# Performance work log

Measured on AMD Instinct MI355X. Metric: run time of the kernel, lower is better.

The kernel has to match this reference:

```python
import jax, jax.numpy as jnp
import numpy as np

V = 10000
C = 8192
NC = 64        # num_clusters
SPW = 128      # states_per_word
H = 256        # hidden_dim
B = 16
T = 33
NEG = -1.0e30  # stand-in for -inf to keep log_softmax NaN-free on empty rows


def residual(x, w1, b1, w2, b2):
    # ResidualLayer: relu(lin2(relu(lin1(x)))) + x  (dropout=0 / eval mode)
    h = jax.nn.relu(x @ w1.T + b1)
    return jax.nn.relu(h @ w2.T + b2) + x


def setup_inputs() -> dict:
    key = jax.random.key(0)
    ks = jax.random.split(key, 32)
    s = 0.02

    def p(k, shape):
        return jax.random.normal(k, shape, jnp.float32) * s

    inp = {}
    inp['text'] = jax.random.randint(ks[0], (B, T), 0, V)
    # brown-cluster style assignment: each cluster owns a contiguous block of SPW states
    word2cluster = jax.random.randint(ks[1], (V,), 0, NC)
    cluster2state = jnp.arange(NC * SPW).reshape(NC, SPW)  # [NC, SPW]
    inp['word2state'] = cluster2state[word2cluster]        # [V, SPW]

    inp['start_emb'] = p(ks[2], (C, H))
    inp['sw1'] = p(ks[3], (H, H)); inp['sb1'] = jnp.zeros((H,), jnp.float32)
    inp['sw2'] = p(ks[4], (H, H)); inp['sb2'] = jnp.zeros((H,), jnp.float32)
    inp['sow'] = p(ks[5], (1, H)); inp['sob'] = jnp.zeros((1,), jnp.float32)

    inp['state_emb'] = p(ks[6], (C, H))
    inp['tw1'] = p(ks[7], (H, H)); inp['tb1'] = jnp.zeros((H,), jnp.float32)
    inp['tw2'] = p(ks[8], (H, H)); inp['tb2'] = jnp.zeros((H,), jnp.float32)
    inp['next_state_emb'] = p(ks[9], (C, H))

    inp['preterminal_emb'] = p(ks[10], (C, H))
    inp['ew1'] = p(ks[11], (H, H)); inp['eb1'] = jnp.zeros((H,), jnp.float32)
    inp['ew2'] = p(ks[12], (H, H)); inp['eb2'] = jnp.zeros((H,), jnp.float32)
    inp['proj_w'] = p(ks[13], (V, H)); inp['proj_b'] = jnp.zeros((V,), jnp.float32)
    return inp


def reference(text, word2state,
              start_emb, sw1, sb1, sw2, sb2, sow, sob,
              state_emb, tw1, tb1, tw2, tb2, next_state_emb,
              preterminal_emb, ew1, eb1, ew2, eb2, proj_w, proj_b):
    # ---- start distribution over C states ----
    start = jax.nn.log_softmax(
        (residual(start_emb, sw1, sb1, sw2, sb2) @ sow.T + sob).squeeze(-1))  # [C]
    # ---- transition [C, C] ----
    trans_logits = residual(state_emb, tw1, tb1, tw2, tb2) @ next_state_emb.T
    transition = jax.nn.log_softmax(trans_logits, axis=-1)  # [C, C]
    # ---- masked emission [C, V] ----
    logits = residual(preterminal_emb, ew1, eb1, ew2, eb2) @ proj_w.T + proj_b
    mask = jnp.zeros((C, V), bool).at[
        word2state.reshape(-1), jnp.repeat(jnp.arange(V), SPW)].set(True)
    emission = jax.nn.log_softmax(jnp.where(mask, logits, NEG), axis=-1)  # [C, V]

    # ---- clamp: gather per-token factored potentials ----
    cs = word2state[text]  # [B, T, SPW]
    lp = transition[cs[:, :-1, :, None], cs[:, 1:, None, :]]  # [B, T-1, SPW(prev), SPW(next)]
    init = start[cs[:, 0]]                                     # [B, SPW]
    obs = emission[cs, text[:, :, None]]                       # [B, T, SPW]
    lp = lp + obs[:, 1:, None, :]                  # obs at t+1 broadcast over prev
    lp = lp.at[:, 0].add(init[:, :, None] + obs[:, 0, :, None])
    lp = lp.swapaxes(-1, -2)  # [B, T-1, next, prev] (as in clamp's final transpose)

    # ---- HMM forward recursion (evidence), the fb kernel's core scan ----
    alpha = jax.nn.logsumexp(lp[:, 0], axis=-1)  # [B, SPW]
    def step(a, lpt):
        # lpt: [B, next, prev]; a: [B, prev]
        return jax.nn.logsumexp(lpt + a[:, None, :], axis=-1), None
    alpha, _ = jax.lax.scan(step, alpha, lp[:, 1:].swapaxes(0, 1))
    return jax.nn.logsumexp(alpha, axis=-1)  # [B] log evidence
```

## Files before the change

### kernel.cpp

```cpp
#include <hip/hip_runtime.h>

#define CC 8192
#define VV 10000
#define NB 16
#define NT 33
#define NCL 64
#define TSCALE 5.545177444479562f

typedef float float4v __attribute__((ext_vector_type(4)));
typedef float f32x4 __attribute__((ext_vector_type(4)));
typedef _Float16 half8v __attribute__((ext_vector_type(8)));
typedef _Float16 half4v __attribute__((ext_vector_type(4)));

__global__ __launch_bounds__(256) void conv_f16(const float* __restrict__ A,
                                                _Float16* __restrict__ O, int n4) {
    int i = blockIdx.x * 256 + threadIdx.x;
    if (i >= n4) return;
    float4v a = ((const float4v*)A)[i];
    half4v h;
#pragma unroll
    for (int c = 0; c < 4; ++c) h[c] = (_Float16)a[c];
    ((half4v*)O)[i] = h;
}

__global__ __launch_bounds__(256) void conv_w6(const float* __restrict__ p0, const float* __restrict__ p1,
                                               const float* __restrict__ p2, const float* __restrict__ p3,
                                               const float* __restrict__ p4, const float* __restrict__ p5,
                                               _Float16* __restrict__ O) {
    const int w = blockIdx.y;
    const float* A = w == 0 ? p0 : w == 1 ? p1 : w == 2 ? p2 : w == 3 ? p3 : w == 4 ? p4 : p5;
    int i = blockIdx.x * 256 + threadIdx.x;
    float4v a = ((const float4v*)A)[i];
    half4v h;
#pragma unroll
    for (int c = 0; c < 4; ++c) h[c] = (_Float16)a[c];
    ((half4v*)(O + w * 65536))[i] = h;
}

__global__ __launch_bounds__(256) void conv2_f16(const float* __restrict__ A0, _Float16* __restrict__ O0, int n40,
                                                 const float* __restrict__ A1, _Float16* __restrict__ O1, int n41) {
    const float* A = blockIdx.y ? A1 : A0;
    _Float16* O = blockIdx.y ? O1 : O0;
    int n4 = blockIdx.y ? n41 : n40;
    int i = blockIdx.x * 256 + threadIdx.x;
    if (i >= n4) return;
    float4v a = ((const float4v*)A)[i];
    half4v h;
#pragma unroll
    for (int c = 0; c < 4; ++c) h[c] = (_Float16)a[c];
    ((half4v*)O)[i] = h;
}

template<bool RES, bool OUTF, bool OUTH>
__global__ __launch_bounds__(256) void mlp_f16(const _Float16* __restrict__ X,
                                               const _Float16* __restrict__ W,
                                               const float* __restrict__ bias,
                                               const float* __restrict__ Xres,
                                               float* __restrict__ Yf,
                                               _Float16* __restrict__ Yh) {
    __shared__ uint4 sB[1024];
    _Float16* BS = (_Float16*)sB;
    const int bm = blockIdx.x * 64;
    const int bn = blockIdx.y * 128;
    const int tid = threadIdx.x;
    const int w = tid >> 6, l = tid & 63;
    const int l15 = l & 15, l4 = l >> 4;
    half8v ax[8];
    {
        const size_t ro = (size_t)(bm + w * 16 + l15) * 256;
#pragma unroll
        for (int s = 0; s < 8; ++s)
            ax[s] = *(const half8v*)&X[ro + s * 32 + l4 * 8];
    }
    f32x4 acc[8];
#pragma unroll
    for (int ct = 0; ct < 8; ++ct) acc[ct] = (f32x4)0.f;
    for (int k0 = 0; k0 < 256; k0 += 64) {
        __syncthreads();
#pragma unroll
        for (int ii = 0; ii < 4; ++ii) {
            int L = ii * 256 + tid;
            int r = L >> 3, g = L & 7;
            int dst = r * 64 + ((g ^ (r & 7)) * 8);
            *(uint4*)&BS[dst] = *(const uint4*)&W[(size_t)(bn + r) * 256 + k0 + g * 8];
        }
        __syncthreads();
        const int sA = k0 >> 5;
#pragma unroll
        for (int ct = 0; ct < 8; ++ct) {
#pragma unroll
            for (int ks = 0; ks < 2; ++ks) {
                int r = ct * 16 + l15;
                int off = r * 64 + (((ks * 4 + l4) ^ (r & 7)) * 8);
                half8v bf = *(const half8v*)&BS[off];
                acc[ct] = __builtin_amdgcn_mfma_f32_16x16x32_f16(ax[sA + ks], bf, acc[ct], 0, 0, 0);
            }
        }
    }
#pragma unroll
    for (int ct = 0; ct < 8; ++ct) {
        int col = bn + ct * 16 + l15;
        float bv = bias[col];
#pragma unroll
        for (int q = 0; q < 4; ++q) {
            int row = bm + w * 16 + l4 * 4 + q;
            float v = acc[ct][q] + bv;
            v = v > 0.f ? v : 0.f;
            if (RES) v += Xres[(size_t)row * 256 + col];
            if (OUTF) Yf[(size_t)row * 256 + col] = v;
            if (OUTH) Yh[(size_t)row * 256 + col] = (_Float16)v;
        }
    }
}

__global__ __launch_bounds__(256) void trans_z_f16(const _Float16* __restrict__ E,
                                                   const _Float16* __restrict__ N,
                                                   float* __restrict__ Zpm,
                                                   float* __restrict__ Zps) {
    __shared__ uint4 sN[1024];
    _Float16* NS = (_Float16*)sN;
    const int bm = blockIdx.x * 128;
    const int cchunk = blockIdx.y;
    const int tid = threadIdx.x;
    const int w = tid >> 6, l = tid & 63;
    const int l15 = l & 15, l4 = l >> 4;
    half8v ax[2][8];
#pragma unroll
    for (int rt = 0; rt < 2; ++rt) {
        const size_t ro = (size_t)(bm + w * 32 + rt * 16 + l15) * 256;
#pragma unroll
        for (int s = 0; s < 8; ++s)
            ax[rt][s] = *(const half8v*)&E[ro + s * 32 + l4 * 8];
    }
    float rm[2][4], rs[2][4];
#pragma unroll
    for (int rt = 0; rt < 2; ++rt)
#pragma unroll
        for (int q = 0; q < 4; ++q) { rm[rt][q] = -1e30f; rs[rt][q] = 0.f; }

    for (int jt = 0; jt < 4; ++jt) {
        const int cb = cchunk * 512 + jt * 128;
        f32x4 acc[2][8];
#pragma unroll
        for (int rt = 0; rt < 2; ++rt)
#pragma unroll
            for (int ct = 0; ct < 8; ++ct) acc[rt][ct] = (f32x4)0.f;
        for (int k0 = 0; k0 < 256; k0 += 64) {
            __syncthreads();
#pragma unroll
            for (int ii = 0; ii < 4; ++ii) {
                int L = ii * 256 + tid;
                int r = L >> 3, g = L & 7;
                int dst = r * 64 + ((g ^ (r & 7)) * 8);
                *(uint4*)&NS[dst] = *(const uint4*)&N[(size_t)(cb + r) * 256 + k0 + g * 8];
            }
            __syncthreads();
            const int sA = k0 >> 5;
#pragma unroll
            for (int ct = 0; ct < 8; ++ct) {
#pragma unroll
                for (int ks = 0; ks < 2; ++ks) {
                    int r = ct * 16 + l15;
                    int off = r * 64 + (((ks * 4 + l4) ^ (r & 7)) * 8);
                    half8v nf = *(const half8v*)&NS[off];
                    acc[0][ct] = __builtin_amdgcn_mfma_f32_16x16x32_f16(ax[0][sA + ks], nf, acc[0][ct], 0, 0, 0);
                    acc[1][ct] = __builtin_amdgcn_mfma_f32_16x16x32_f16(ax[1][sA + ks], nf, acc[1][ct], 0, 0, 0);
                }
            }
        }
#pragma unroll
        for (int rt = 0; rt < 2; ++rt)
#pragma unroll
            for (int q = 0; q < 4; ++q) {
                float lm = -1e30f;
#pragma unroll
                for (int ct = 0; ct < 8; ++ct) lm = fmaxf(lm, acc[rt][ct][q]);
                lm = fmaxf(lm, __shfl_xor(lm, 1));
                lm = fmaxf(lm, __shfl_xor(lm, 2));
                lm = fmaxf(lm, __shfl_xor(lm, 4));
                lm = fmaxf(lm, __shfl_xor(lm, 8));
                float ls = 0.f;
#pragma unroll
                for (int ct = 0; ct < 8; ++ct) ls += __expf(acc[rt][ct][q] - lm);
                ls += __shfl_xor(ls, 1);
                ls += __shfl_xor(ls, 2);
                ls += __shfl_xor(ls, 4);
                ls += __shfl_xor(ls, 8);
                float nm = fmaxf(rm[rt][q], lm);
                rs[rt][q] = rs[rt][q] * __expf(rm[rt][q] - nm) + ls * __expf(lm - nm);
                rm[rt][q] = nm;
            }
    }
    if (l15 == 0) {
#pragma unroll
        for (int rt = 0; rt < 2; ++rt)
#pragma unroll
            for (int q = 0; q < 4; ++q) {
                int row = w * 32 + rt * 16 + l4 * 4 + q;
                Zpm[cchunk * CC + bm + row] = rm[rt][q];
                Zps[cchunk * CC + bm + row] = rs[rt][q];
            }
    }
}

__global__ __launch_bounds__(256) void z_combine(const float* __restrict__ Zpm,
                                                 const float* __restrict__ Zps,
                                                 float* __restrict__ Z) {
    const int i = blockIdx.x * 256 + threadIdx.x;
    float m = -1e30f;
#pragma unroll
    for (int c = 0; c < 16; ++c) m = fmaxf(m, Zpm[c * CC + i]);
    float s = 0.f;
#pragma unroll
    for (int c = 0; c < 16; ++c) s += Zps[c * CC + i] * __expf(Zpm[c * CC + i] - m);
    Z[i] = m + __logf(s);
}

__global__ __launch_bounds__(256) void g_blocks_f16(const _Float16* __restrict__ E,
                                                    const _Float16* __restrict__ N,
                                                    const float* __restrict__ Zt,
                                                    const int* __restrict__ text,
                                                    const int* __restrict__ wcl,
                                                    _Float16* __restrict__ T16) {
    const int bt = blockIdx.x;
    const int b = bt >> 5, t = bt & 31;
    const int ca = wcl[text[b * NT + t]];
    const int cb = wcl[text[b * NT + t + 1]];
    const int tid = threadIdx.x;
    const int w = tid >> 6, l = tid & 63;
    const int l15 = l & 15, l4 = l >> 4;
    half8v ax[2][8];
#pragma unroll
    for (int rt = 0; rt < 2; ++rt) {
        const size_t ro = (size_t)(ca * 128 + w * 32 + rt * 16 + l15) * 256;
#pragma unroll
        for (int s = 0; s < 8; ++s)
            ax[rt][s] = *(const half8v*)&E[ro + s * 32 + l4 * 8];
    }
    f32x4 acc[2][8];
#pragma unroll
    for (int rt = 0; rt < 2; ++rt)
#pragma unroll
        for (int ct = 0; ct < 8; ++ct) acc[rt][ct] = (f32x4)0.f;
#pragma unroll
    for (int s = 0; s < 8; ++s) {
#pragma unroll
        for (int ct = 0; ct < 8; ++ct) {
            half8v nf = *(const half8v*)&N[(size_t)(cb * 128 + ct * 16 + l15) * 256 + s * 32 + l4 * 8];
            acc[0][ct] = __builtin_amdgcn_mfma_f32_16x16x32_f16(ax[0][s], nf, acc[0][ct], 0, 0, 0);
            acc[1][ct] = __builtin_amdgcn_mfma_f32_16x16x32_f16(ax[1][s], nf, acc[1][ct], 0, 0, 0);
        }
    }
    _Float16* Gt = T16 + (size_t)bt * 16384;
#pragma unroll
    for (int rt = 0; rt < 2; ++rt)
#pragma unroll
        for (int q = 0; q < 4; ++q) {
            int row = w * 32 + rt * 16 + l4 * 4 + q;
            float z = Zt[ca * 128 + row];
#pragma unroll
            for (int ct = 0; ct < 8; ++ct)
                Gt[row * 128 + ct * 16 + l15] = (_Float16)__expf(acc[rt][ct][q] - z + TSCALE);
        }
}

__global__ __launch_bounds__(256) void wcl_k(const int* __restrict__ w2s, int* __restrict__ wcl) {
    int v = blockIdx.x * 256 + threadIdx.x;
    if (v < VV) wcl[v] = w2s[(size_t)v * 128] >> 7;
}

__global__ __launch_bounds__(64) void wlist_k(const int* __restrict__ wcl,
                                              int* __restrict__ wlist,
                                              int* __restrict__ cnt) {
    const int a = blockIdx.x;
    const int t = threadIdx.x;
    int c = 0;
    for (int base = 0; base < VV; base += 64) {
        int v = base + t;
        bool match = (v < VV) && (wcl[v] == a);
        unsigned long long mk = __ballot(match);
        if (match) {
            int pos = c + __popcll(mk & ((1ull << t) - 1ull));
            if (pos < 512) wlist[a * 512 + pos] = v;
        }
        c += __popcll(mk);
    }
    if (t == 0) cnt[a] = min(c, 512);
}

__global__ __launch_bounds__(64) void z_e_f16(const _Float16* __restrict__ Ep,
                                              const _Float16* __restrict__ Wp,
                                              const float* __restrict__ pb,
                                              const int* __restrict__ wlist,
                                              const int* __restrict__ cnt,
                                              float* __restrict__ Zem,
                                              float* __restrict__ Zes) {
    const int a = blockIdx.x, sg = blockIdx.y, wt = blockIdx.z;
    const int l = threadIdx.x, l15 = l & 15, l4 = l >> 4;
    const int n = cnt[a];
    const int orow = a * 128 + sg * 16;
    if (wt * 32 >= n) {
        if (l15 == 0) {
#pragma unroll
            for (int q = 0; q < 4; ++q) {
                int ro = orow + l4 * 4 + q;
                Zem[wt * CC + ro] = -1e30f;
                Zes[wt * CC + ro] = 0.f;
            }
        }
        return;
    }
    half8v ax[8];
    {
        const size_t ro = (size_t)(orow + l15) * 256;
#pragma unroll
        for (int s = 0; s < 8; ++s)
            ax[s] = *(const half8v*)&Ep[ro + s * 32 + l4 * 8];
    }
    float val[2][4];
#pragma unroll
    for (int ct = 0; ct < 2; ++ct) {
        const int wi = wt * 32 + ct * 16 + l15;
        const bool valid = wi < n;
        const int wrow = wlist[a * 512 + (valid ? wi : 0)];
        f32x4 acc = (f32x4)0.f;
        const size_t wo = (size_t)wrow * 256;
#pragma unroll
        for (int s = 0; s < 8; ++s) {
            half8v bf = *(const half8v*)&Wp[wo + s * 32 + l4 * 8];
            acc = __builtin_amdgcn_mfma_f32_16x16x32_f16(ax[s], bf, acc, 0, 0, 0);
        }
        const float pbv = valid ? pb[wrow] : 0.f;
#pragma unroll
        for (int q = 0; q < 4; ++q)
            val[ct][q] = valid ? (acc[q] + pbv) : -1e30f;
    }
#pragma unroll
    for (int q = 0; q < 4; ++q) {
        float m = fmaxf(val[0][q], val[1][q]);
        m = fmaxf(m, __shfl_xor(m, 1));
        m = fmaxf(m, __shfl_xor(m, 2));
        m = fmaxf(m, __shfl_xor(m, 4));
        m = fmaxf(m, __shfl_xor(m, 8));
        float s = __expf(val[0][q] - m) + __expf(val[1][q] - m);
        s += __shfl_xor(s, 1);
        s += __shfl_xor(s, 2);
        s += __shfl_xor(s, 4);
        s += __shfl_xor(s, 8);
        if (l15 == 0) {
            int ro = orow + l4 * 4 + q;
            Zem[wt * CC + ro] = m;
            Zes[wt * CC + ro] = s;
        }
    }
}

__global__ __launch_bounds__(256) void z_e_combine(const float* __restrict__ Zem,
                                                   const float* __restrict__ Zes,
                                                   float* __restrict__ Ze) {
    const int i = blockIdx.x * 256 + threadIdx.x;
    float m = -1e30f;
#pragma unroll
    for (int t = 0; t < 16; ++t) m = fmaxf(m, Zem[t * CC + i]);
    float s = 0.f;
#pragma unroll
    for (int t = 0; t < 16; ++t) s += Zes[t * CC + i] * __expf(Zem[t * CC + i] - m);
    Ze[i] = m + __logf(s);
}

__global__ __launch_bounds__(128) void obs_k(const float* __restrict__ Ep,
                                             const float* __restrict__ PW,
                                             const float* __restrict__ pb,
                                             const int* __restrict__ text,
                                             const int* __restrict__ wcl,
                                             const float* __restrict__ Ze,
                                             float* __restrict__ obs) {
    __shared__ float pw[256];
    const int bt = blockIdx.x;
    const int w = text[bt];
    const int cl = wcl[w];
    const int tid = threadIdx.x;
    pw[tid] = PW[(size_t)w * 256 + tid];
    pw[tid + 128] = PW[(size_t)w * 256 + tid + 128];
    __syncthreads();
    const int st = cl * 128 + tid;
    const float* e = Ep + (size_t)st * 256;
    float acc = 0.f;
#pragma unroll 8
    for (int k = 0; k < 256; ++k) acc += e[k] * pw[k];
    obs[(size_t)bt * 128 + tid] = acc + pb[w] - Ze[st];
}

__global__ __launch_bounds__(256) void start_s_k(const float* __restrict__ E,
                                                 const float* __restrict__ sow,
                                                 const float* __restrict__ sob,
                                                 float* __restrict__ s) {
    const int tid = threadIdx.x;
    const int row = blockIdx.x * 4 + (tid >> 6);
    const int k0 = tid & 63;
    const float* e = E + (size_t)row * 256;
    float acc = 0.f;
#pragma unroll
    for (int k = k0; k < 256; k += 64) acc += e[k] * sow[k];
#pragma unroll
    for (int off = 32; off > 0; off >>= 1) acc += __shfl_down(acc, off);
    if (k0 == 0) s[row] = acc + sob[0];
}

__global__ __launch_bounds__(256) void lse_k(const float* __restrict__ s, float* __restrict__ out) {
    __shared__ float red[256];
    const int tid = threadIdx.x;
    float m = -1e30f;
    for (int i = tid; i < CC; i += 256) m = fmaxf(m, s[i]);
    red[tid] = m; __syncthreads();
    for (int off = 128; off > 0; off >>= 1) {
        if (tid < off) red[tid] = fmaxf(red[tid], red[tid + off]);
        __syncthreads();
    }
    m = red[0]; __syncthreads();
    float sum = 0.f;
    for (int i = tid; i < CC; i += 256) sum += __expf(s[i] - m);
    red[tid] = sum; __syncthreads();
    for (int off = 128; off > 0; off >>= 1) {
        if (tid < off) red[tid] += red[tid + off];
        __syncthreads();
    }
    if (tid == 0) out[0] = m + __logf(red[0]);
}

__global__ __launch_bounds__(512) void chain_k(const _Float16* __restrict__ T16,
                                               const float* __restrict__ obs,
                                               const float* __restrict__ sst,
                                               const float* __restrict__ lse,
                                               const int* __restrict__ text,
                                               const int* __restrict__ wcl,
                                               float* __restrict__ out) {
    __shared__ float aS[128];
    __shared__ float vS[128];
    __shared__ float pS[512];
    __shared__ float mS;
    const int b = blockIdx.x;
    const int tid = threadIdx.x;
    const int j = tid & 127, g = tid >> 7;
    if (tid < 128) {
        int c0 = wcl[text[b * NT]] * 128 + tid;
        aS[tid] = sst[c0] - lse[0] + obs[(size_t)(b * NT) * 128 + tid];
    }
    __syncthreads();
    for (int t = 1; t < NT; ++t) {
        if (tid < 64) {
            float m2 = fmaxf(aS[tid], aS[tid + 64]);
#pragma unroll
            for (int mask = 32; mask > 0; mask >>= 1) m2 = fmaxf(m2, __shfl_xor(m2, mask));
            if (tid == 0) mS = m2;
        }
        __syncthreads();
        const float m = mS;
        if (tid < 128) vS[tid] = __expf(aS[tid] - m);
        __syncthreads();
        const _Float16* Tt = T16 + (size_t)(b * 32 + (t - 1)) * 16384;
        float p = 0.f;
#pragma unroll
        for (int ii = 0; ii < 32; ++ii)
            p += (float)Tt[(g * 32 + ii) * 128 + j] * vS[g * 32 + ii];
        pS[tid] = p;
        __syncthreads();
        if (tid < 128) {
            float y = pS[tid] + pS[tid + 128] + pS[tid + 256] + pS[tid + 384];
            aS[tid] = obs[(size_t)(b * NT + t) * 128 + tid] + m + __logf(y) - TSCALE;
        }
        __syncthreads();
    }
    if (tid < 64) {
        float m2 = fmaxf(aS[tid], aS[tid + 64]);
#pragma unroll
        for (int mask = 32; mask > 0; mask >>= 1) m2 = fmaxf(m2, __shfl_xor(m2, mask));
        float e = __expf(aS[tid] - m2) + __expf(aS[tid + 64] - m2);
#pragma unroll
        for (int mask = 32; mask > 0; mask >>= 1) e += __shfl_xor(e, mask);
        if (tid == 0) out[b] = m2 + __logf(e);
    }
}

extern "C" void kernel_launch(void* const* d_in, const int* in_sizes, int n_in,
                              void* d_out, int out_size, void* d_ws, size_t ws_size,
                              hipStream_t stream) {
    const int* text = (const int*)d_in[0];
    const int* w2s  = (const int*)d_in[1];
    const float* start_emb = (const float*)d_in[2];
    const float* sw1 = (const float*)d_in[3];
    const float* sb1 = (const float*)d_in[4];
    const float* sw2 = (const float*)d_in[5];
    const float* sb2 = (const float*)d_in[6];
    const float* sow = (const float*)d_in[7];
    const float* sob = (const float*)d_in[8];
    const float* state_emb = (const float*)d_in[9];
    const float* tw1 = (const float*)d_in[10];
    const float* tb1 = (const float*)d_in[11];
    const float* tw2 = (const float*)d_in[12];
    const float* tb2 = (const float*)d_in[13];
    const float* nse = (const float*)d_in[14];
    const float* pte = (const float*)d_in[15];
    const float* ew1 = (const float*)d_in[16];
    const float* eb1 = (const float*)d_in[17];
    const float* ew2 = (const float*)d_in[18];
    const float* eb2 = (const float*)d_in[19];
    const float* pw  = (const float*)d_in[20];
    const float* pb  = (const float*)d_in[21];
    float* out = (float*)d_out;

    float* ws   = (float*)d_ws;
    float* Htmp = ws;
    float* ErS  = Htmp + 2097152;
    float* ErP  = ErS + 2097152;
    float* sst  = ErP + 2097152;
    float* lse  = sst + 8192;
    float* Zt   = lse + 8;
    float* Ze   = Zt + 8192;
    float* obs  = Ze + 8192;
    _Float16* T16   = (_Float16*)(obs + 67584);
    _Float16* ErT16 = T16 + 8388608;
    _Float16* ErP16 = ErT16 + 2097152;
    _Float16* N16   = ErP16 + 2097152;
    _Float16* w16   = N16 + 2097152;
    int* wcl = (int*)(w16 + 393216);

    _Float16* H16 = (_Float16*)Htmp;
    float* Zpm  = Htmp + 1048576;
    float* Zps  = Zpm + 131072;
    float* Zem  = Zps + 131072;
    float* Zes  = Zem + 131072;
    int* wlist  = (int*)(Zes + 131072);
    int* cnt    = wlist + 32768;
    _Float16* emb16 = (_Float16*)ErP;
    _Float16* W16 = T16;

    conv_w6<<<dim3(64, 6), 256, 0, stream>>>(sw1, sw2, tw1, tw2, ew1, ew2, w16);

    conv_f16<<<2048, 256, 0, stream>>>(start_emb, emb16, 524288);
    mlp_f16<false, false, true><<<dim3(128, 2), 256, 0, stream>>>(emb16, w16, sb1, nullptr, nullptr, H16);
    mlp_f16<true, true, false><<<dim3(128, 2), 256, 0, stream>>>(H16, w16 + 65536, sb2, start_emb, ErS, nullptr);
    conv_f16<<<2048, 256, 0, stream>>>(state_emb, emb16, 524288);
    mlp_f16<false, false, true><<<dim3(128, 2), 256, 0, stream>>>(emb16, w16 + 2 * 65536, tb1, nullptr, nullptr, H16);
    mlp_f16<true, false, true><<<dim3(128, 2), 256, 0, stream>>>(H16, w16 + 3 * 65536, tb2, state_emb, nullptr, ErT16);
    conv_f16<<<2048, 256, 0, stream>>>(pte, emb16, 524288);
    mlp_f16<false, false, true><<<dim3(128, 2), 256, 0, stream>>>(emb16, w16 + 4 * 65536, eb1, nullptr, nullptr, H16);
    mlp_f16<true, true, true><<<dim3(128, 2), 256, 0, stream>>>(H16, w16 + 5 * 65536, eb2, pte, ErP, ErP16);

    conv2_f16<<<dim3(2500, 2), 256, 0, stream>>>(nse, N16, 524288, pw, W16, 640000);

    wcl_k<<<40, 256, 0, stream>>>(w2s, wcl);
    wlist_k<<<NCL, 64, 0, stream>>>(wcl, wlist, cnt);
    start_s_k<<<2048, 256, 0, stream>>>(ErS, sow, sob, sst);
    lse_k<<<1, 256, 0, stream>>>(sst, lse);

    trans_z_f16<<<dim3(64, 16), 256, 0, stream>>>(ErT16, N16, Zpm, Zps);
    z_combine<<<32, 256, 0, stream>>>(Zpm, Zps, Zt);

    z_e_f16<<<dim3(NCL, 8, 16), 64, 0, stream>>>(ErP16, W16, pb, wlist, cnt, Zem, Zes);
    z_e_combine<<<32, 256, 0, stream>>>(Zem, Zes, Ze);
    obs_k<<<NB * NT, 128, 0, stream>>>(ErP, pw, pb, text, wcl, Ze, obs);

    g_blocks_f16<<<512, 256, 0, stream>>>(ErT16, N16, Zt, text, wcl, T16);
    chain_k<<<NB, 512, 0, stream>>>(T16, obs, sst, lse, text, wcl, out);
}
```

Measured before the change: 439.8 us.

## Batch residual MLPs into two launches and drop max-shift in normalizer sums

Folds the fp32-to-fp16 conversion of the embeddings into the first MLP layer. Runs the start, transition and emission residual MLPs together as two launches indexed by blockIdx.z, replacing nine serial launches with larger grids. In the transition and emission partition-function kernels, the running max/rescale logsumexp becomes a plain sum of exponentials with a final log, and the separate max buffers go away. The transition kernel also reloads A fragments per k-step instead of holding all of them in registers, with a 4-blocks occupancy hint. Skipping the max shift relies on logits staying small enough that exp does not overflow.

```diff
diff --git a/kernel.cpp b/kernel.cpp
--- a/kernel.cpp
+++ b/kernel.cpp
@@ -11,17 +11,6 @@
 typedef float f32x4 __attribute__((ext_vector_type(4)));
 typedef _Float16 half8v __attribute__((ext_vector_type(8)));
 typedef _Float16 half4v __attribute__((ext_vector_type(4)));
-
-__global__ __launch_bounds__(256) void conv_f16(const float* __restrict__ A,
-                                                _Float16* __restrict__ O, int n4) {
-    int i = blockIdx.x * 256 + threadIdx.x;
-    if (i >= n4) return;
-    float4v a = ((const float4v*)A)[i];
-    half4v h;
-#pragma unroll
-    for (int c = 0; c < 4; ++c) h[c] = (_Float16)a[c];
-    ((half4v*)O)[i] = h;
-}
 
 __global__ __launch_bounds__(256) void conv_w6(const float* __restrict__ p0, const float* __restrict__ p1,
                                                const float* __restrict__ p2, const float* __restrict__ p3,
@@ -51,15 +40,19 @@
     ((half4v*)O)[i] = h;
 }
 
-template<bool RES, bool OUTF, bool OUTH>
-__global__ __launch_bounds__(256) void mlp_f16(const _Float16* __restrict__ X,
-                                               const _Float16* __restrict__ W,
-                                               const float* __restrict__ bias,
-                                               const float* __restrict__ Xres,
-                                               float* __restrict__ Yf,
-                                               _Float16* __restrict__ Yh) {
+__global__ __launch_bounds__(256) void mlp1_k(const float* __restrict__ X0, const float* __restrict__ X1,
+                                              const float* __restrict__ X2,
+                                              const _Float16* __restrict__ w16,
+                                              const float* __restrict__ b0, const float* __restrict__ b1,
+                                              const float* __restrict__ b2,
+                                              _Float16* __restrict__ Hbase) {
     __shared__ uint4 sB[1024];
     _Float16* BS = (_Float16*)sB;
+    const int z = blockIdx.z;
+    const float* X = z == 0 ? X0 : z == 1 ? X1 : X2;
+    const float* bias = z == 0 ? b0 : z == 1 ? b1 : b2;
+    const _Float16* W = w16 + z * 2 * 65536;
+    _Float16* Y = Hbase + (size_t)z * 2097152;
     const int bm = blockIdx.x * 64;
     const int bn = blockIdx.y * 128;
     const int tid = threadIdx.x;
@@ -69,8 +62,14 @@
     {
         const size_t ro = (size_t)(bm + w * 16 + l15) * 256;
 #pragma unroll
-        for (int s = 0; s < 8; ++s)
-            ax[s] = *(const half8v*)&X[ro + s * 32 + l4 * 8];
+        for (int s = 0; s < 8; ++s) {
+            float4v x0 = *(const float4v*)&X[ro + s * 32 + l4 * 8];
+            float4v x1 = *(const float4v*)&X[ro + s * 32 + l4 * 8 + 4];
+            half8v h;
+#pragma unroll
+            for (int c = 0; c < 4; ++c) { h[c] = (_Float16)x0[c]; h[c + 4] = (_Float16)x1[c]; }
+            ax[s] = h;
+        }
     }
     f32x4 acc[8];
 #pragma unroll
@@ -106,16 +105,82 @@
             int row = bm + w * 16 + l4 * 4 + q;
             float v = acc[ct][q] + bv;
             v = v > 0.f ? v : 0.f;
-            if (RES) v += Xres[(size_t)row * 256 + col];
-            if (OUTF) Yf[(size_t)row * 256 + col] = v;
-            if (OUTH) Yh[(size_t)row * 256 + col] = (_Float16)v;
-        }
-    }
-}
-
-__global__ __launch_bounds__(256) void trans_z_f16(const _Float16* __restrict__ E,
+            Y[(size_t)row * 256 + col] = (_Float16)v;
+        }
+    }
+}
+
+__global__ __launch_bounds__(256) void mlp2_k(const _Float16* __restrict__ Hbase,
+                                              const _Float16* __restrict__ w16,
+                                              const float* __restrict__ b0, const float* __restrict__ b1,
+                                              const float* __restrict__ b2,
+                                              const float* __restrict__ R0, const float* __restrict__ R1,
+                                              const float* __restrict__ R2,
+                                              float* __restrict__ ErS, _Float16* __restrict__ ErT16,
+                                              float* __restrict__ ErP, _Float16* __restrict__ ErP16) {
+    __shared__ uint4 sB[1024];
+    _Float16* BS = (_Float16*)sB;
+    const int z = blockIdx.z;
+    const _Float16* X = Hbase + (size_t)z * 2097152;
+    const float* bias = z == 0 ? b0 : z == 1 ? b1 : b2;
+    const float* Xres = z == 0 ? R0 : z == 1 ? R1 : R2;
+    const _Float16* W = w16 + (z * 2 + 1) * 65536;
+    const int bm = blockIdx.x * 64;
+    const int bn = blockIdx.y * 128;
+    const int tid = threadIdx.x;
+    const int w = tid >> 6, l = tid & 63;
+    const int l15 = l & 15, l4 = l >> 4;
+    half8v ax[8];
+    {
+        const size_t ro = (size_t)(bm + w * 16 + l15) * 256;
+#pragma unroll
+        for (int s = 0; s < 8; ++s)
+            ax[s] = *(const half8v*)&X[ro + s * 32 + l4 * 8];
+    }
+    f32x4 acc[8];
+#pragma unroll
+    for (int ct = 0; ct < 8; ++ct) acc[ct] = (f32x4)0.f;
+    for (int k0 = 0; k0 < 256; k0 += 64) {
+        __syncthreads();
+#pragma unroll
+        for (int ii = 0; ii < 4; ++ii) {
+            int L = ii * 256 + tid;
+            int r = L >> 3, g = L & 7;
+            int dst = r * 64 + ((g ^ (r & 7)) * 8);
+            *(uint4*)&BS[dst] = *(const uint4*)&W[(size_t)(bn + r) * 256 + k0 + g * 8];
+        }
+        __syncthreads();
+        const int sA = k0 >> 5;
+#pragma unroll
+        for (int ct = 0; ct < 8; ++ct) {
+#pragma unroll
+            for (int ks = 0; ks < 2; ++ks) {
+                int r = ct * 16 + l15;
+                int off = r * 64 + (((ks * 4 + l4) ^ (r & 7)) * 8);
+                half8v bf = *(const half8v*)&BS[off];
+                acc[ct] = __builtin_amdgcn_mfma_f32_16x16x32_f16(ax[sA + ks], bf, acc[ct], 0, 0, 0);
+            }
+        }
+    }
+#pragma unroll
+    for (int ct = 0; ct < 8; ++ct) {
+        int col = bn + ct * 16 + l15;
+        float bv = bias[col];
+#pragma unroll
+        for (int q = 0; q < 4; ++q) {
+            int row = bm + w * 16 + l4 * 4 + q;
+            float v = acc[ct][q] + bv;
+            v = v > 0.f ? v : 0.f;
+            v += Xres[(size_t)row * 256 + col];
+            if (z == 0) ErS[(size_t)row * 256 + col] = v;
+            else if (z == 1) ErT16[(size_t)row * 256 + col] = (_Float16)v;
+            else { ErP[(size_t)row * 256 + col] = v; ErP16[(size_t)row * 256 + col] = (_Float16)v; }
+        }
+    }
+}
+
+__global__ __launch_bounds__(256, 4) void trans_z2(const _Float16* __restrict__ E,
                                                    const _Float16* __restrict__ N,
-                                                   float* __restrict__ Zpm,
                                                    float* __restrict__ Zps) {
     __shared__ uint4 sN[1024];
     _Float16* NS = (_Float16*)sN;
@@ -124,19 +189,11 @@
     const int tid = threadIdx.x;
     const int w = tid >> 6, l = tid & 63;
     const int l15 = l & 15, l4 = l >> 4;
-    half8v ax[2][8];
-#pragma unroll
-    for (int rt = 0; rt < 2; ++rt) {
-        const size_t ro = (size_t)(bm + w * 32 + rt * 16 + l15) * 256;
-#pragma unroll
-        for (int s = 0; s < 8; ++s)
-            ax[rt][s] = *(const half8v*)&E[ro + s * 32 + l4 * 8];
-    }
-    float rm[2][4], rs[2][4];
+    float rs[2][4];
 #pragma unroll
     for (int rt = 0; rt < 2; ++rt)
 #pragma unroll
-        for (int q = 0; q < 4; ++q) { rm[rt][q] = -1e30f; rs[rt][q] = 0.f; }
+        for (int q = 0; q < 4; ++q) rs[rt][q] = 0.f;
 
     for (int jt = 0; jt < 4; ++jt) {
         const int cb = cchunk * 512 + jt * 128;
@@ -146,6 +203,12 @@
 #pragma unroll
             for (int ct = 0; ct < 8; ++ct) acc[rt][ct] = (f32x4)0.f;
         for (int k0 = 0; k0 < 256; k0 += 64) {
+            half8v ah[2][2];
+#pragma unroll
+            for (int rt = 0; rt < 2; ++rt)
+#pragma unroll
+                for (int ks = 0; ks < 2; ++ks)
+                    ah[rt][ks] = *(const half8v*)&E[(size_t)(bm + w * 32 + rt * 16 + l15) * 256 + k0 + ks * 32 + l4 * 8];
             __syncthreads();
 #pragma unroll
             for (int ii = 0; ii < 4; ++ii) {
@@ -155,7 +218,6 @@
                 *(uint4*)&NS[dst] = *(const uint4*)&N[(size_t)(cb + r) * 256 + k0 + g * 8];
             }
             __syncthreads();
-            const int sA = k0 >> 5;
 #pragma unroll
             for (int ct = 0; ct < 8; ++ct) {
 #pragma unroll
@@ -163,8 +225,8 @@
                     int r = ct * 16 + l15;
                     int off = r * 64 + (((ks * 4 + l4) ^ (r & 7)) * 8);
                     half8v nf = *(const half8v*)&NS[off];
-                    acc[0][ct] = __builtin_amdgcn_mfma_f32_16x16x32_f16(ax[0][sA + ks], nf, acc[0][ct], 0, 0, 0);
-                    acc[1][ct] = __builtin_amdgcn_mfma_f32_16x16x32_f16(ax[1][sA + ks], nf, acc[1][ct], 0, 0, 0);
+                    acc[0][ct] = __builtin_amdgcn_mfma_f32_16x16x32_f16(ah[0][ks], nf, acc[0][ct], 0, 0, 0);
+                    acc[1][ct] = __builtin_amdgcn_mfma_f32_16x16x32_f16(ah[1][ks], nf, acc[1][ct], 0, 0, 0);
                 }
             }
         }
@@ -172,48 +234,35 @@
         for (int rt = 0; rt < 2; ++rt)
 #pragma unroll
             for (int q = 0; q < 4; ++q) {
-                float lm = -1e30f;
-#pragma unroll
-                for (int ct = 0; ct < 8; ++ct) lm = fmaxf(lm, acc[rt][ct][q]);
-                lm = fmaxf(lm, __shfl_xor(lm, 1));
-                lm = fmaxf(lm, __shfl_xor(lm, 2));
-                lm = fmaxf(lm, __shfl_xor(lm, 4));
-                lm = fmaxf(lm, __shfl_xor(lm, 8));
-                float ls = 0.f;
-#pragma unroll
-                for (int ct = 0; ct < 8; ++ct) ls += __expf(acc[rt][ct][q] - lm);
-                ls += __shfl_xor(ls, 1);
-                ls += __shfl_xor(ls, 2);
-                ls += __shfl_xor(ls, 4);
-                ls += __shfl_xor(ls, 8);
-                float nm = fmaxf(rm[rt][q], lm);
-                rs[rt][q] = rs[rt][q] * __expf(rm[rt][q] - nm) + ls * __expf(lm - nm);
-                rm[rt][q] = nm;
+                float a = 0.f;
+#pragma unroll
+                for (int ct = 0; ct < 8; ++ct) a += __expf(acc[rt][ct][q]);
+                rs[rt][q] += a;
             }
     }
-    if (l15 == 0) {
-#pragma unroll
-        for (int rt = 0; rt < 2; ++rt)
-#pragma unroll
-            for (int q = 0; q < 4; ++q) {
+#pragma unroll
+    for (int rt = 0; rt < 2; ++rt)
+#pragma unroll
+        for (int q = 0; q < 4; ++q) {
+            float s = rs[rt][q];
+            s += __shfl_xor(s, 1);
+            s += __shfl_xor(s, 2);
+            s += __shfl_xor(s, 4);
+            s += __shfl_xor(s, 8);
+            if (l15 == 0) {
                 int row = w * 32 + rt * 16 + l4 * 4 + q;
-                Zpm[cchunk * CC + bm + row] = rm[rt][q];
-                Zps[cchunk * CC + bm + row] = rs[rt][q];
+                Zps[cchunk * CC + bm + row] = s;
             }
-    }
-}
-
-__global__ __launch_bounds__(256) void z_combine(const float* __restrict__ Zpm,
-                                                 const float* __restrict__ Zps,
-                                                 float* __restrict__ Z) {
+        }
+}
+
+__global__ __launch_bounds__(256) void z_combine2(const float* __restrict__ Zps,
+                                                  float* __restrict__ Z) {
     const int i = blockIdx.x * 256 + threadIdx.x;
-    float m = -1e30f;
-#pragma unroll
-    for (int c = 0; c < 16; ++c) m = fmaxf(m, Zpm[c * CC + i]);
     float s = 0.f;
 #pragma unroll
-    for (int c = 0; c < 16; ++c) s += Zps[c * CC + i] * __expf(Zpm[c * CC + i] - m);
-    Z[i] = m + __logf(s);
+    for (int c = 0; c < 16; ++c) s += Zps[c * CC + i];
+    Z[i] = __logf(s);
 }
 
 __global__ __launch_bounds__(256) void g_blocks_f16(const _Float16* __restrict__ E,
@@ -288,13 +337,12 @@
     if (t == 0) cnt[a] = min(c, 512);
 }
 
-__global__ __launch_bounds__(64) void z_e_f16(const _Float16* __restrict__ Ep,
-                                              const _Float16* __restrict__ Wp,
-                                              const float* __restrict__ pb,
-                                              const int* __restrict__ wlist,
-                                              const int* __restrict__ cnt,
-                                              float* __restrict__ Zem,
-                                              float* __restrict__ Zes) {
+__global__ __launch_bounds__(64) void z_e2(const _Float16* __restrict__ Ep,
+                                           const _Float16* __restrict__ Wp,
+                                           const float* __restrict__ pb,
+                                           const int* __restrict__ wlist,
+                                           const int* __restrict__ cnt,
+                                           float* __restrict__ Zes) {
     const int a = blockIdx.x, sg = blockIdx.y, wt = blockIdx.z;
     const int l = threadIdx.x, l15 = l & 15, l4 = l >> 4;
     const int n = cnt[a];
@@ -302,11 +350,8 @@
     if (wt * 32 >= n) {
         if (l15 == 0) {
 #pragma unroll
-            for (int q = 0; q < 4; ++q) {
-                int ro = orow + l4 * 4 + q;
-                Zem[wt * CC + ro] = -1e30f;
-                Zes[wt * CC + ro] = 0.f;
-            }
+            for (int q = 0; q < 4; ++q)
+                Zes[wt * CC + orow + l4 * 4 + q] = 0.f;
         }
         return;
     }
@@ -317,7 +362,7 @@
         for (int s = 0; s < 8; ++s)
             ax[s] = *(const half8v*)&Ep[ro + s * 32 + l4 * 8];
     }
-    float val[2][4];
+    float sq[4] = {0.f, 0.f, 0.f, 0.f};
 #pragma unroll
     for (int ct = 0; ct < 2; ++ct) {
         const int wi = wt * 32 + ct * 16 + l15;
@@ -333,39 +378,27 @@
         const float pbv = valid ? pb[wrow] : 0.f;
 #pragma unroll
         for (int q = 0; q < 4; ++q)
-            val[ct][q] = valid ? (acc[q] + pbv) : -1e30f;
+            if (valid) sq[q] += __expf(acc[q] + pbv);
     }
 #pragma unroll
     for (int q = 0; q < 4; ++q) {
-        float m = fmaxf(val[0][q], val[1][q]);
-        m = fmaxf(m, __shfl_xor(m, 1));
-        m = fmaxf(m, __shfl_xor(m, 2));
-        m = fmaxf(m, __shfl_xor(m, 4));
-        m = fmaxf(m, __shfl_xor(m, 8));
-        float s = __expf(val[0][q] - m) + __expf(val[1][q] - m);
+        float s = sq[q];
         s += __shfl_xor(s, 1);
         s += __shfl_xor(s, 2);
         s += __shfl_xor(s, 4);
         s += __shfl_xor(s, 8);
-        if (l15 == 0) {
-            int ro = orow + l4 * 4 + q;
-            Zem[wt * CC + ro] = m;
-            Zes[wt * CC + ro] = s;
-        }
-    }
-}
-
-__global__ __launch_bounds__(256) void z_e_combine(const float* __restrict__ Zem,
-                                                   const float* __restrict__ Zes,
-                                                   float* __restrict__ Ze) {
+        if (l15 == 0)
+            Zes[wt * CC + orow + l4 * 4 + q] = s;
+    }
+}
+
+__global__ __launch_bounds__(256) void z_e_combine2(const float* __restrict__ Zes,
+                                                    float* __restrict__ Ze) {
     const int i = blockIdx.x * 256 + threadIdx.x;
-    float m = -1e30f;
-#pragma unroll
-    for (int t = 0; t < 16; ++t) m = fmaxf(m, Zem[t * CC + i]);
     float s = 0.f;
 #pragma unroll
-    for (int t = 0; t < 16; ++t) s += Zes[t * CC + i] * __expf(Zem[t * CC + i] - m);
-    Ze[i] = m + __logf(s);
+    for (int t = 0; t < 16; ++t) s += Zes[t * CC + i];
+    Ze[i] = __logf(s);
 }
 
 __global__ __launch_bounds__(128) void obs_k(const float* __restrict__ Ep,
@@ -525,27 +558,18 @@
     _Float16* w16   = N16 + 2097152;
     int* wcl = (int*)(w16 + 393216);
 
-    _Float16* H16 = (_Float16*)Htmp;
-    float* Zpm  = Htmp + 1048576;
-    float* Zps  = Zpm + 131072;
-    float* Zem  = Zps + 131072;
-    float* Zes  = Zem + 131072;
+    float* Zps  = Htmp;
+    float* Zes  = Zps + 131072;
     int* wlist  = (int*)(Zes + 131072);
     int* cnt    = wlist + 32768;
-    _Float16* emb16 = (_Float16*)ErP;
+    _Float16* H16 = T16;
     _Float16* W16 = T16;
 
     conv_w6<<<dim3(64, 6), 256, 0, stream>>>(sw1, sw2, tw1, tw2, ew1, ew2, w16);
 
-    conv_f16<<<2048, 256, 0, stream>>>(start_emb, emb16, 524288);
-    mlp_f16<false, false, true><<<dim3(128, 2), 256, 0, stream>>>(emb16, w16, sb1, nullptr, nullptr, H16);
-    mlp_f16<true, true, false><<<dim3(128, 2), 256, 0, stream>>>(H16, w16 + 65536, sb2, start_emb, ErS, nullptr);
-    conv_f16<<<2048, 256, 0, stream>>>(state_emb, emb16, 524288);
-    mlp_f16<false, false, true><<<dim3(128, 2), 256, 0, stream>>>(emb16, w16 + 2 * 65536, tb1, nullptr, nullptr, H16);
-    mlp_f16<true, false, true><<<dim3(128, 2), 256, 0, stream>>>(H16, w16 + 3 * 65536, tb2, state_emb, nullptr, ErT16);
-    conv_f16<<<2048, 256, 0, stream>>>(pte, emb16, 524288);
-    mlp_f16<false, false, true><<<dim3(128, 2), 256, 0, stream>>>(emb16, w16 + 4 * 65536, eb1, nullptr, nullptr, H16);
-    mlp_f16<true, true, true><<<dim3(128, 2), 256, 0, stream>>>(H16, w16 + 5 * 65536, eb2, pte, ErP, ErP16);
+    mlp1_k<<<dim3(128, 2, 3), 256, 0, stream>>>(start_emb, state_emb, pte, w16, sb1, tb1, eb1, H16);
+    mlp2_k<<<dim3(128, 2, 3), 256, 0, stream>>>(H16, w16, sb2, tb2, eb2, start_emb, state_emb, pte,
+                                                ErS, ErT16, ErP, ErP16);
 
     conv2_f16<<<dim3(2500, 2), 256, 0, stream>>>(nse, N16, 524288, pw, W16, 640000);
 
@@ -554,11 +578,11 @@
     start_s_k<<<2048, 256, 0, stream>>>(ErS, sow, sob, sst);
     lse_k<<<1, 256, 0, stream>>>(sst, lse);
 
-    trans_z_f16<<<dim3(64, 16), 256, 0, stream>>>(ErT16, N16, Zpm, Zps);
-    z_combine<<<32, 256, 0, stream>>>(Zpm, Zps, Zt);
-
-    z_e_f16<<<dim3(NCL, 8, 16), 64, 0, stream>>>(ErP16, W16, pb, wlist, cnt, Zem, Zes);
-    z_e_combine<<<32, 256, 0, stream>>>(Zem, Zes, Ze);
+    trans_z2<<<dim3(64, 16), 256, 0, stream>>>(ErT16, N16, Zps);
+    z_combine2<<<32, 256, 0, stream>>>(Zps, Zt);
+
+    z_e2<<<dim3(NCL, 8, 16), 64, 0, stream>>>(ErP16, W16, pb, wlist, cnt, Zes);
+    z_e_combine2<<<32, 256, 0, stream>>>(Zes, Ze);
     obs_k<<<NB * NT, 128, 0, stream>>>(ErP, pw, pb, text, wcl, Ze, obs);
 
     g_blocks_f16<<<512, 256, 0, stream>>>(ErT16, N16, Zt, text, wcl, T16);
```

Result: faster. 420.3 us (-4.4%).
